# Optimization experiments

Measured on AMD Instinct MI355X. Metric: run time of the kernel, lower is better.

The kernel has to match this reference:

```python
import jax, jax.numpy as jnp
import numpy as np

DIM = 1536
HEADS = 12
HEAD_DIM = DIM // HEADS
EPS = 1e-6
IMG_LEN = 257


def _rmsnorm(x, g):
    var = jnp.mean(jnp.square(x), axis=-1, keepdims=True)
    return x * jax.lax.rsqrt(var + EPS) * g


def _attn(q, k, v):
    # q: [b, Lq, h, d], k/v: [b, Lk, h, d]
    scale = 1.0 / jnp.sqrt(jnp.asarray(HEAD_DIM, q.dtype))
    s = jnp.einsum('bqhd,bkhd->bhqk', q, k) * scale
    p = jax.nn.softmax(s, axis=-1)
    return jnp.einsum('bhqk,bkhd->bqhd', p, v)


def setup_inputs() -> dict:
    key = jax.random.key(0)
    ks = jax.random.split(key, 20)
    w = lambda k: jax.random.normal(k, (DIM, DIM), dtype=jnp.float32) * 0.02
    b = lambda k: jax.random.normal(k, (DIM,), dtype=jnp.float32) * 0.01
    return {
        'x': jax.random.normal(ks[0], (1, 16384, DIM), dtype=jnp.float32),
        'context': jax.random.normal(ks[1], (1, 769, DIM), dtype=jnp.float32),
        'context_lens': jax.random.randint(ks[2], (1,), 0, 512, dtype=jnp.int32),
        'Wq': w(ks[3]), 'bq': b(ks[4]),
        'Wk': w(ks[5]), 'bk': b(ks[6]),
        'Wv': w(ks[7]), 'bv': b(ks[8]),
        'W_addk': w(ks[9]), 'b_addk': b(ks[10]),
        'W_addv': w(ks[11]), 'b_addv': b(ks[12]),
        'Wo': w(ks[13]), 'bo': b(ks[14]),
        'gq': jnp.ones((DIM,), dtype=jnp.float32),
        'gk': jnp.ones((DIM,), dtype=jnp.float32),
        'g_addk': jnp.ones((DIM,), dtype=jnp.float32),
    }


def reference(x, context, context_lens, Wq, bq, Wk, bk, Wv, bv,
              W_addk, b_addk, W_addv, b_addv, Wo, bo, gq, gk, g_addk):
    b_sz, L1, _ = x.shape
    ctx_img = context[:, :IMG_LEN]   # [B, 257, C]
    ctx_txt = context[:, IMG_LEN:]   # [B, L2-257, C]

    q = _rmsnorm(x @ Wq + bq, gq).reshape(b_sz, -1, HEADS, HEAD_DIM)
    k = _rmsnorm(ctx_txt @ Wk + bk, gk).reshape(b_sz, -1, HEADS, HEAD_DIM)
    v = (ctx_txt @ Wv + bv).reshape(b_sz, -1, HEADS, HEAD_DIM)
    k_img = _rmsnorm(ctx_img @ W_addk + b_addk, g_addk).reshape(b_sz, -1, HEADS, HEAD_DIM)
    v_img = (ctx_img @ W_addv + b_addv).reshape(b_sz, -1, HEADS, HEAD_DIM)

    img_x = _attn(q, k_img, v_img).reshape(b_sz, L1, DIM)
    txt_x = _attn(q, k, v).reshape(b_sz, L1, DIM)
    out = (txt_x + img_x) @ Wo + bo
    return out
```

## Files before the change

kernel.cpp:

```cpp
#include <hip/hip_runtime.h>
#include <cstdint>
#include <cstddef>

typedef unsigned short u16;
typedef unsigned int u32;
typedef short bfrag __attribute__((ext_vector_type(8)));
typedef __bf16 yfrag __attribute__((ext_vector_type(8)));
typedef float f4 __attribute__((ext_vector_type(4)));

__device__ __forceinline__ u16 f2bs(float f) {
  union { float f; u32 u; } x; x.f = f;
  u32 r = x.u + 0x7fffu + ((x.u >> 16) & 1u);
  return (u16)(r >> 16);
}
__device__ __forceinline__ float bs2f(u16 s) {
  union { u32 u; float f; } x; x.u = ((u32)s) << 16;
  return x.f;
}
__device__ __forceinline__ u32 cvtpk_bf16(float lo, float hi) {
  u32 d;
  asm("v_cvt_pk_bf16_f32 %0, %1, %2" : "=v"(d) : "v"(lo), "v"(hi));
  return d;
}

template <typename T>
__device__ __forceinline__ auto mfma_sel(T a, T b, f4 c, int)
    -> decltype(__builtin_amdgcn_mfma_f32_16x16x32_bf16(a, b, c, 0, 0, 0)) {
  return __builtin_amdgcn_mfma_f32_16x16x32_bf16(a, b, c, 0, 0, 0);
}
template <typename T>
__device__ __forceinline__ f4 mfma_sel(T a, T b, f4 c, long) {
  yfrag ya = __builtin_bit_cast(yfrag, a);
  yfrag yb = __builtin_bit_cast(yfrag, b);
  return __builtin_amdgcn_mfma_f32_16x16x32_bf16(ya, yb, c, 0, 0, 0);
}
__device__ __forceinline__ f4 MFMA(bfrag a, bfrag b, f4 c) {
  return mfma_sel(a, b, c, 0);
}

__device__ __forceinline__ void gl2lds16(const u16* g, u16* l) {
  __builtin_amdgcn_global_load_lds(
      (__attribute__((address_space(1))) void*)(g),
      (__attribute__((address_space(3))) void*)(l), 16, 0, 0);
}

__global__ __launch_bounds__(256) void cvt2(const float* __restrict__ x,
                                            u16* __restrict__ xbf,
                                            const float* __restrict__ ctx,
                                            u16* __restrict__ ctxb) {
  int i = blockIdx.x * 256 + threadIdx.x;
  const float* src; u16* dst;
  if (i < 3145728) {
    src = x; dst = xbf;
  } else {
    i -= 3145728;
    if (i >= 147648) return;
    src = ctx; dst = ctxb;
  }
  const float4* s4 = (const float4*)src;
  float4 a = s4[(size_t)i * 2];
  float4 b = s4[(size_t)i * 2 + 1];
  uint4 o;
  o.x = cvtpk_bf16(a.x, a.y);
  o.y = cvtpk_bf16(a.z, a.w);
  o.z = cvtpk_bf16(b.x, b.y);
  o.w = cvtpk_bf16(b.z, b.w);
  ((uint4*)dst)[i] = o;
}

__global__ __launch_bounds__(256) void transpose6(
    const float* s0, const float* s1, const float* s2, const float* s3,
    const float* s4, const float* s5, u16* d0, u16* d1, u16* d2, u16* d3,
    u16* d4, u16* d5) {
  const float* src; u16* dst;
  switch (blockIdx.z) {
    case 0: src = s0; dst = d0; break;
    case 1: src = s1; dst = d1; break;
    case 2: src = s2; dst = d2; break;
    case 3: src = s3; dst = d3; break;
    case 4: src = s4; dst = d4; break;
    default: src = s5; dst = d5; break;
  }
  __shared__ float tile[32][33];
  int tx = threadIdx.x, ty = threadIdx.y;
  int bx = blockIdx.x * 32, by = blockIdx.y * 32;
#pragma unroll
  for (int j = 0; j < 4; j++)
    tile[ty + j * 8][tx] = src[(size_t)(by + ty + j * 8) * 1536 + bx + tx];
  __syncthreads();
#pragma unroll
  for (int j = 0; j < 4; j++)
    dst[(size_t)(bx + ty + j * 8) * 1536 + by + tx] = f2bs(tile[tx][ty + j * 8]);
}

__device__ __forceinline__ void gemm256_core(
    const u16* __restrict__ A, const u16* __restrict__ Bt,
    const float* __restrict__ bias, void* __restrict__ outp,
    int Mreal, int ldT, int epi, int bx, int by, u16* As, u16* Bs) {
  const int tid = threadIdx.x;
  const int w = tid >> 6, lane = tid & 63;
  const int quad = lane >> 4, l15 = lane & 15;
  const int wm = w >> 2, wn = w & 3;
  const int m0 = bx * 256, n0 = by * 256;

  f4 acc[8][4];
#pragma unroll
  for (int i = 0; i < 8; i++)
#pragma unroll
    for (int j = 0; j < 4; j++) acc[i][j] = f4{0.f, 0.f, 0.f, 0.f};

  const int rbase = w * 8 + (lane >> 3);
  const int csrc = ((lane & 7) ^ (lane >> 3)) * 8;
  const u16* Ab = A + (size_t)m0 * 1536;
  const u16* Bb = Bt + (size_t)n0 * 1536;

#define STG(Gb, Ls, t)                                                      \
  {                                                                         \
    u16* d_ = (Ls) + ((t) & 1) * 16384;                                     \
    const u16* s_ = (Gb) + (size_t)(t) * 64 + csrc;                         \
    _Pragma("unroll")                                                       \
    for (int j = 0; j < 4; j++)                                             \
      gl2lds16(s_ + (size_t)(j * 64 + rbase) * 1536,                        \
               d_ + (j * 512 + w * 64) * 8);                                \
  }

  STG(Ab, As, 0); STG(Bb, Bs, 0);
  STG(Ab, As, 1); STG(Bb, Bs, 1);

  for (int kt = 0; kt < 24; ++kt) {
    const u16* Asb = As + (kt & 1) * 16384;
    const u16* Bsb = Bs + (kt & 1) * 16384;
    if (kt < 23)
      asm volatile("s_waitcnt vmcnt(8)\n\ts_barrier" ::: "memory");
    else
      asm volatile("s_waitcnt vmcnt(0)\n\ts_barrier" ::: "memory");

    bfrag af[8], bf[4];
#pragma unroll
    for (int nf = 0; nf < 4; nf++) {
      const int R = wn * 64 + nf * 16 + l15;
      bf[nf] = *(const bfrag*)(Bsb + R * 64 + ((quad ^ (R & 7)) * 8));
    }
#pragma unroll
    for (int mf = 0; mf < 8; mf++) {
      const int R = wm * 128 + mf * 16 + l15;
      af[mf] = *(const bfrag*)(Asb + R * 64 + ((quad ^ (R & 7)) * 8));
    }
    __builtin_amdgcn_s_setprio(1);
#pragma unroll
    for (int mf = 0; mf < 8; mf++)
#pragma unroll
      for (int nf = 0; nf < 4; nf++)
        acc[mf][nf] = MFMA(af[mf], bf[nf], acc[mf][nf]);
    __builtin_amdgcn_s_setprio(0);

    bfrag af1[8], bf1[4];
#pragma unroll
    for (int nf = 0; nf < 4; nf++) {
      const int R = wn * 64 + nf * 16 + l15;
      bf1[nf] = *(const bfrag*)(Bsb + R * 64 + (((4 + quad) ^ (R & 7)) * 8));
    }
#pragma unroll
    for (int mf = 0; mf < 8; mf++) {
      const int R = wm * 128 + mf * 16 + l15;
      af1[mf] = *(const bfrag*)(Asb + R * 64 + (((4 + quad) ^ (R & 7)) * 8));
    }
    asm volatile("s_waitcnt lgkmcnt(0)\n\ts_barrier" ::: "memory");
    if (kt < 22) { STG(Ab, As, kt + 2); STG(Bb, Bs, kt + 2); }
    __builtin_amdgcn_s_setprio(1);
#pragma unroll
    for (int mf = 0; mf < 8; mf++)
#pragma unroll
      for (int nf = 0; nf < 4; nf++)
        acc[mf][nf] = MFMA(af1[mf], bf1[nf], acc[mf][nf]);
    __builtin_amdgcn_s_setprio(0);
  }
#undef STG

  float bcol[4];
#pragma unroll
  for (int nf = 0; nf < 4; nf++) bcol[nf] = bias[n0 + wn * 64 + nf * 16 + l15];

  if (epi == 1) {
    u16* dst = (u16*)outp;
#pragma unroll
    for (int mf = 0; mf < 8; mf++)
#pragma unroll
      for (int r = 0; r < 4; r++) {
        int row = m0 + wm * 128 + mf * 16 + quad * 4 + r;
        if (row < Mreal) {
#pragma unroll
          for (int nf = 0; nf < 4; nf++) {
            int col = n0 + wn * 64 + nf * 16 + l15;
            dst[(size_t)col * ldT + row] = f2bs(acc[mf][nf][r] + bcol[nf]);
          }
        }
      }
  } else if (epi == 0) {
    u16* dst = (u16*)outp;
#pragma unroll
    for (int mf = 0; mf < 8; mf++)
#pragma unroll
      for (int r = 0; r < 4; r++) {
        int row = m0 + wm * 128 + mf * 16 + quad * 4 + r;
        if (row < Mreal) {
#pragma unroll
          for (int nf = 0; nf < 4; nf++) {
            int col = n0 + wn * 64 + nf * 16 + l15;
            dst[(size_t)row * 1536 + col] = f2bs(acc[mf][nf][r] + bcol[nf]);
          }
        }
      }
  } else {
    float* dst = (float*)outp;
#pragma unroll
    for (int mf = 0; mf < 8; mf++)
#pragma unroll
      for (int r = 0; r < 4; r++) {
        int row = m0 + wm * 128 + mf * 16 + quad * 4 + r;
        if (row < Mreal) {
#pragma unroll
          for (int nf = 0; nf < 4; nf++) {
            int col = n0 + wn * 64 + nf * 16 + l15;
            dst[(size_t)row * 1536 + col] = acc[mf][nf][r] + bcol[nf];
          }
        }
      }
  }
}

__global__ __launch_bounds__(512, 2) void gemm256(
    const u16* __restrict__ xbf, const u16* __restrict__ wqT,
    const float* __restrict__ bq, u16* __restrict__ qb,
    const u16* __restrict__ ctxb, const u16* __restrict__ wkT,
    const float* __restrict__ bk, u16* __restrict__ ktxt,
    const u16* __restrict__ wakT, const float* __restrict__ bak,
    u16* __restrict__ kimg, const u16* __restrict__ wvT,
    const float* __restrict__ bv, u16* __restrict__ vtt,
    const u16* __restrict__ wavT, const float* __restrict__ bav,
    u16* __restrict__ vti, const u16* __restrict__ yb,
    const u16* __restrict__ woT, const float* __restrict__ bo,
    float* __restrict__ out, int mode) {
  extern __shared__ u16 lds[];
  u16* As = lds;
  u16* Bs = lds + 32768;
  const int cpx = gridDim.x >> 3;
  int id = (blockIdx.x & 7) * cpx + (blockIdx.x >> 3);
  const u16* ctxt = ctxb + 257 * 1536;
  const u16* A; const u16* Bt; const float* bias; void* outp;
  int Mreal, ldT, epi, bx, by;
  if (mode == 1) {
    A = yb; Bt = woT; bias = bo; outp = out;
    Mreal = 16384; ldT = 0; epi = 2; bx = id & 63; by = id >> 6;
  } else if (id < 384) {
    A = xbf; Bt = wqT; bias = bq; outp = qb;
    Mreal = 16384; ldT = 0; epi = 0; bx = id & 63; by = id >> 6;
  } else if (id < 396) {
    int t = id - 384;
    A = ctxt; Bt = wkT; bias = bk; outp = ktxt;
    Mreal = 512; ldT = 0; epi = 0; bx = t & 1; by = t >> 1;
  } else if (id < 408) {
    int t = id - 396;
    A = ctxb; Bt = wakT; bias = bak; outp = kimg;
    Mreal = 257; ldT = 0; epi = 0; bx = t & 1; by = t >> 1;
  } else if (id < 420) {
    int t = id - 408;
    A = ctxt; Bt = wvT; bias = bv; outp = vtt;
    Mreal = 512; ldT = 512; epi = 1; bx = t & 1; by = t >> 1;
  } else {
    int t = id - 420;
    A = ctxb; Bt = wavT; bias = bav; outp = vti;
    Mreal = 257; ldT = 264; epi = 1; bx = t & 1; by = t >> 1;
  }
  gemm256_core(A, Bt, bias, outp, Mreal, ldT, epi, bx, by, As, Bs);
}

__global__ __launch_bounds__(256) void rmsnorm_multi(
    u16* __restrict__ qb, const float* __restrict__ gq,
    u16* __restrict__ ktxt, const float* __restrict__ gk,
    u16* __restrict__ kimg, const float* __restrict__ gak) {
  int row = blockIdx.x;
  u16* buf; const float* g;
  if (row < 16384) {
    buf = qb; g = gq;
  } else if (row < 16896) {
    buf = ktxt; g = gk; row -= 16384;
  } else {
    buf = kimg; g = gak; row -= 16896;
  }
  const int tid = threadIdx.x;
  u32* p = (u32*)(buf + (size_t)row * 1536);
  const float2* g2 = (const float2*)g;
  u32 d[3];
  float v[6];
  float ss = 0.f;
#pragma unroll
  for (int j = 0; j < 3; j++) {
    d[j] = p[tid + j * 256];
    v[2 * j]     = bs2f((u16)(d[j] & 0xffffu));
    v[2 * j + 1] = bs2f((u16)(d[j] >> 16));
    ss += v[2 * j] * v[2 * j] + v[2 * j + 1] * v[2 * j + 1];
  }
#pragma unroll
  for (int off = 32; off; off >>= 1) ss += __shfl_xor(ss, off);
  __shared__ float red[4];
  if ((tid & 63) == 0) red[tid >> 6] = ss;
  __syncthreads();
  ss = red[0] + red[1] + red[2] + red[3];
  const float sc = rsqrtf(ss * (1.0f / 1536.0f) + 1e-6f);
#pragma unroll
  for (int j = 0; j < 3; j++) {
    float2 gg = g2[tid + j * 256];
    p[tid + j * 256] =
        cvtpk_bf16(v[2 * j] * sc * gg.x, v[2 * j + 1] * sc * gg.y);
  }
}

#define ATTN_SCALE 0.08838834764831845f
__global__ __launch_bounds__(256, 2) void attn_kernel(
    const u16* __restrict__ q, const u16* __restrict__ ktxt,
    const u16* __restrict__ kimg, const u16* __restrict__ vttxt,
    const u16* __restrict__ vtimg, u16* __restrict__ y) {
  __shared__ u16 Ks[64 * 128];
  __shared__ u16 Vs[128 * 64];
  __shared__ u16 Ps[4 * 32 * 72];
  const int tid = threadIdx.x;
  const int w = tid >> 6, lane = tid & 63;
  const int quad = lane >> 4, l15 = lane & 15;
  const int h = blockIdx.y, hoff = h * 128;
  const int mw = blockIdx.x * 128 + w * 32;
  u16* Pw = Ps + w * (32 * 72);

  bfrag qf[2][4];
#pragma unroll
  for (int rt = 0; rt < 2; rt++) {
    const u16* qrow = q + (size_t)(mw + rt * 16 + l15) * 1536 + hoff + quad * 8;
#pragma unroll
    for (int c = 0; c < 4; c++) qf[rt][c] = *(const bfrag*)(qrow + c * 32);
  }

  int kko[4], kco[4], vfe[4], vco[4];
#pragma unroll
  for (int j = 0; j < 4; j++) {
    int i = j * 256 + tid;
    int s = i >> 4, cp = i & 15;
    kko[j] = 4 * (s & 15) + (s >> 4);
    kco[j] = ((cp ^ (s & 7)) * 8);
    int f = i >> 3, cq = i & 7;
    vfe[j] = f;
    vco[j] = ((cq ^ (f & 7)) * 8);
  }

  f4 o[2][8];
  u32 resA[2][8][2];
  float lr[2][4];

  for (int seg = 0; seg < 2; seg++) {
    const u16* kp = seg ? ktxt : kimg;
    const u16* vp = seg ? vttxt : vtimg;
    const int Lk = seg ? 512 : 257;
    const int ldv = seg ? 512 : 264;
    const int nit = seg ? 8 : 5;
#pragma unroll
    for (int rt = 0; rt < 2; rt++) {
#pragma unroll
      for (int ft = 0; ft < 8; ft++) o[rt][ft] = f4{0.f, 0.f, 0.f, 0.f};
#pragma unroll
      for (int r = 0; r < 4; r++) lr[rt][r] = 0.f;
    }

    for (int it = 0; it < nit; ++it) {
      const int t0 = it * 64;
#pragma unroll
      for (int j = 0; j < 4; j++)
        gl2lds16(kp + (size_t)(t0 + kko[j]) * 1536 + hoff + kco[j],
                 Ks + (j * 256 + w * 64) * 8);
#pragma unroll
      for (int j = 0; j < 4; j++)
        gl2lds16(vp + (size_t)(hoff + vfe[j]) * ldv + t0 + vco[j],
                 Vs + (j * 256 + w * 64) * 8);
      __syncthreads();

      f4 s[2][4];
#pragma unroll
      for (int rt = 0; rt < 2; rt++)
#pragma unroll
        for (int t = 0; t < 4; t++) s[rt][t] = f4{0.f, 0.f, 0.f, 0.f};
#pragma unroll
      for (int t = 0; t < 4; t++) {
        const u16* kb = Ks + (t * 16 + l15) * 128;
        bfrag kf[4];
#pragma unroll
        for (int c = 0; c < 4; c++)
          kf[c] = *(const bfrag*)(kb + (((c * 4 + quad) ^ (l15 & 7)) * 8));
#pragma unroll
        for (int rt = 0; rt < 2; rt++)
#pragma unroll
          for (int c = 0; c < 4; c++)
            s[rt][t] = MFMA(qf[rt][c], kf[c], s[rt][t]);
      }

      if (t0 + 64 <= Lk) {
#pragma unroll
        for (int rt = 0; rt < 2; rt++)
#pragma unroll
          for (int t = 0; t < 4; t++)
#pragma unroll
            for (int r = 0; r < 4; r++) {
              float p = __expf(s[rt][t][r] * ATTN_SCALE);
              s[rt][t][r] = p;
              lr[rt][r] += p;
            }
      } else {
#pragma unroll
        for (int t = 0; t < 4; t++) {
          bool ok = (t0 + 4 * l15 + t) < Lk;
#pragma unroll
          for (int rt = 0; rt < 2; rt++)
#pragma unroll
            for (int r = 0; r < 4; r++) {
              float p = ok ? __expf(s[rt][t][r] * ATTN_SCALE) : 0.f;
              s[rt][t][r] = p;
              lr[rt][r] += p;
            }
        }
      }

#pragma unroll
      for (int rt = 0; rt < 2; rt++)
#pragma unroll
        for (int r = 0; r < 4; r++) {
          u32 lo = cvtpk_bf16(s[rt][0][r], s[rt][1][r]);
          u32 hi = cvtpk_bf16(s[rt][2][r], s[rt][3][r]);
          *(uint2*)(Pw + (rt * 16 + quad * 4 + r) * 72 + l15 * 4) =
              make_uint2(lo, hi);
        }
      asm volatile("s_waitcnt lgkmcnt(0)" ::: "memory");
      bfrag pf[2][2];
#pragma unroll
      for (int rt = 0; rt < 2; rt++)
#pragma unroll
        for (int hf = 0; hf < 2; hf++)
          pf[rt][hf] =
              *(const bfrag*)(Pw + (rt * 16 + l15) * 72 + hf * 32 + quad * 8);

#pragma unroll
      for (int ft = 0; ft < 8; ft++) {
        const u16* vb = Vs + (ft * 16 + l15) * 64;
#pragma unroll
        for (int hf = 0; hf < 2; hf++) {
          bfrag vf = *(const bfrag*)(vb + (((hf * 4 + quad) ^ (l15 & 7)) * 8));
#pragma unroll
          for (int rt = 0; rt < 2; rt++)
            o[rt][ft] = MFMA(pf[rt][hf], vf, o[rt][ft]);
        }
      }
      __syncthreads();
    }

#pragma unroll
    for (int rt = 0; rt < 2; rt++)
#pragma unroll
      for (int r = 0; r < 4; r++) {
        float v = lr[rt][r];
        v += __shfl_xor(v, 1);
        v += __shfl_xor(v, 2);
        v += __shfl_xor(v, 4);
        v += __shfl_xor(v, 8);
        lr[rt][r] = 1.0f / v;
      }
    if (seg == 0) {
#pragma unroll
      for (int rt = 0; rt < 2; rt++)
#pragma unroll
        for (int ft = 0; ft < 8; ft++) {
          resA[rt][ft][0] = cvtpk_bf16(o[rt][ft][0] * lr[rt][0],
                                       o[rt][ft][1] * lr[rt][1]);
          resA[rt][ft][1] = cvtpk_bf16(o[rt][ft][2] * lr[rt][2],
                                       o[rt][ft][3] * lr[rt][3]);
        }
    }
  }

#pragma unroll
  for (int rt = 0; rt < 2; rt++)
#pragma unroll
    for (int ft = 0; ft < 8; ft++) {
      float ra[4];
      ra[0] = bs2f((u16)(resA[rt][ft][0] & 0xffffu));
      ra[1] = bs2f((u16)(resA[rt][ft][0] >> 16));
      ra[2] = bs2f((u16)(resA[rt][ft][1] & 0xffffu));
      ra[3] = bs2f((u16)(resA[rt][ft][1] >> 16));
#pragma unroll
      for (int r = 0; r < 4; r++)
        y[(size_t)(mw + rt * 16 + quad * 4 + r) * 1536 + hoff + ft * 16 + l15] =
            f2bs(ra[r] + o[rt][ft][r] * lr[rt][r]);
    }
}

extern "C" void kernel_launch(void* const* d_in, const int* in_sizes, int n_in,
                              void* d_out, int out_size, void* d_ws,
                              size_t ws_size, hipStream_t stream) {
  const float* x   = (const float*)d_in[0];
  const float* ctx = (const float*)d_in[1];
  const float* Wq  = (const float*)d_in[3];
  const float* bq  = (const float*)d_in[4];
  const float* Wk  = (const float*)d_in[5];
  const float* bk  = (const float*)d_in[6];
  const float* Wv  = (const float*)d_in[7];
  const float* bv  = (const float*)d_in[8];
  const float* Wak = (const float*)d_in[9];
  const float* bak = (const float*)d_in[10];
  const float* Wav = (const float*)d_in[11];
  const float* bav = (const float*)d_in[12];
  const float* Wo  = (const float*)d_in[13];
  const float* bo  = (const float*)d_in[14];
  const float* gq  = (const float*)d_in[15];
  const float* gk  = (const float*)d_in[16];
  const float* gak = (const float*)d_in[17];
  float* out = (float*)d_out;

  u16* xbf  = (u16*)d_ws;
  u16* qb   = xbf + 25165824;
  u16* ctxb = qb + 25165824;
  u16* wqT  = ctxb + 1181184;
  u16* wkT  = wqT + 2359296;
  u16* wvT  = wkT + 2359296;
  u16* wakT = wvT + 2359296;
  u16* wavT = wakT + 2359296;
  u16* woT  = wavT + 2359296;
  u16* ktxt = woT + 2359296;
  u16* kimg = ktxt + 786432;
  u16* vti  = kimg + 394752;
  u16* vtt  = vti + 405504;

  cvt2<<<12865, 256, 0, stream>>>(x, xbf, ctx, ctxb);
  transpose6<<<dim3(48, 48, 6), dim3(32, 8), 0, stream>>>(
      Wq, Wk, Wv, Wak, Wav, Wo, wqT, wkT, wvT, wakT, wavT, woT);

  gemm256<<<432, 512, 131072, stream>>>(xbf, wqT, bq, qb,
                                        ctxb, wkT, bk, ktxt,
                                        wakT, bak, kimg,
                                        wvT, bv, vtt,
                                        wavT, bav, vti,
                                        xbf, woT, bo, out, 0);

  rmsnorm_multi<<<17153, 256, 0, stream>>>(qb, gq, ktxt, gk, kimg, gak);

  attn_kernel<<<dim3(128, 12), 256, 0, stream>>>(qb, ktxt, kimg, vtt, vti, xbf);

  gemm256<<<384, 512, 131072, stream>>>(xbf, wqT, bq, qb,
                                        ctxb, wkT, bk, ktxt,
                                        wakT, bak, kimg,
                                        wvT, bv, vtt,
                                        wavT, bav, vti,
                                        xbf, woT, bo, out, 1);
}
```

Before: 575.9 us.

## Restructure 256x256 GEMM mainloop into 4-stage BK=32 pipeline with split staging

The GEMM main loop moves from a double-buffered BK=64 scheme to a quadruple-buffered BK=32 scheme with three tiles in flight. A and B global-to-LDS loads are interleaved between two half-MFMA phases, and the LDS layout and swizzle are reorganised to match. The wait and barrier schedule is rewritten per iteration to keep more loads outstanding. Launch bounds drop to one block per SM, which frees registers but may lower occupancy, and the extra barriers per iteration add synchronisation overhead.

Result: slower. 590.6 us (+2.5%).

```diff
diff --git a/kernel.cpp b/kernel.cpp
--- a/kernel.cpp
+++ b/kernel.cpp
@@ -109,71 +109,80 @@
 #pragma unroll
     for (int j = 0; j < 4; j++) acc[i][j] = f4{0.f, 0.f, 0.f, 0.f};
 
-  const int rbase = w * 8 + (lane >> 3);
-  const int csrc = ((lane & 7) ^ (lane >> 3)) * 8;
+  const int g = lane >> 3;
+  const int c_ = (lane & 7) ^ g;
+  const int R0 = (c_ >> 2) * 128 + w * 8 + g;
+  const int qs = (c_ & 3) * 8;
   const u16* Ab = A + (size_t)m0 * 1536;
   const u16* Bb = Bt + (size_t)n0 * 1536;
 
-#define STG(Gb, Ls, t)                                                      \
-  {                                                                         \
-    u16* d_ = (Ls) + ((t) & 1) * 16384;                                     \
-    const u16* s_ = (Gb) + (size_t)(t) * 64 + csrc;                         \
-    _Pragma("unroll")                                                       \
-    for (int j = 0; j < 4; j++)                                             \
-      gl2lds16(s_ + (size_t)(j * 64 + rbase) * 1536,                        \
-               d_ + (j * 512 + w * 64) * 8);                                \
+#define STG(Gb, Ls, t)                                                     \
+  {                                                                        \
+    u16* d_ = (Ls) + ((t) & 3) * 8192;                                     \
+    const u16* s_ = (Gb) + (size_t)(t) * 32 + qs;                          \
+    gl2lds16(s_ + (size_t)R0 * 1536, d_ + (w * 64) * 8);                   \
+    gl2lds16(s_ + (size_t)(R0 + 64) * 1536, d_ + (512 + w * 64) * 8);      \
   }
 
   STG(Ab, As, 0); STG(Bb, Bs, 0);
   STG(Ab, As, 1); STG(Bb, Bs, 1);
-
-  for (int kt = 0; kt < 24; ++kt) {
-    const u16* Asb = As + (kt & 1) * 16384;
-    const u16* Bsb = Bs + (kt & 1) * 16384;
-    if (kt < 23)
-      asm volatile("s_waitcnt vmcnt(8)\n\ts_barrier" ::: "memory");
-    else
-      asm volatile("s_waitcnt vmcnt(0)\n\ts_barrier" ::: "memory");
-
-    bfrag af[8], bf[4];
+  STG(Ab, As, 2); STG(Bb, Bs, 2);
+  asm volatile("s_waitcnt vmcnt(8)" ::: "memory");
+  __builtin_amdgcn_s_barrier();
+
+  for (int kt = 0; kt < 48; ++kt) {
+    const u16* Asb = As + (kt & 3) * 8192;
+    const u16* Bsb = Bs + (kt & 3) * 8192;
+
+    bfrag bf[4], af[4];
 #pragma unroll
     for (int nf = 0; nf < 4; nf++) {
-      const int R = wn * 64 + nf * 16 + l15;
-      bf[nf] = *(const bfrag*)(Bsb + R * 64 + ((quad ^ (R & 7)) * 8));
-    }
-#pragma unroll
-    for (int mf = 0; mf < 8; mf++) {
-      const int R = wm * 128 + mf * 16 + l15;
-      af[mf] = *(const bfrag*)(Asb + R * 64 + ((quad ^ (R & 7)) * 8));
-    }
+      const int br = (wn & 1) * 64 + nf * 16 + l15;
+      bf[nf] = *(const bfrag*)(Bsb + br * 64 +
+                               ((((wn >> 1) * 4 + quad) ^ (br & 7)) * 8));
+    }
+#pragma unroll
+    for (int mf = 0; mf < 4; mf++) {
+      const int ar = mf * 16 + l15;
+      af[mf] = *(const bfrag*)(Asb + ar * 64 +
+                               (((wm * 4 + quad) ^ (ar & 7)) * 8));
+    }
+    if (kt < 45) STG(Ab, As, kt + 3);
+    __builtin_amdgcn_s_barrier();
+    asm volatile("s_waitcnt lgkmcnt(0)" ::: "memory");
     __builtin_amdgcn_s_setprio(1);
 #pragma unroll
-    for (int mf = 0; mf < 8; mf++)
+    for (int mf = 0; mf < 4; mf++)
 #pragma unroll
       for (int nf = 0; nf < 4; nf++)
         acc[mf][nf] = MFMA(af[mf], bf[nf], acc[mf][nf]);
     __builtin_amdgcn_s_setprio(0);
-
-    bfrag af1[8], bf1[4];
-#pragma unroll
-    for (int nf = 0; nf < 4; nf++) {
-      const int R = wn * 64 + nf * 16 + l15;
-      bf1[nf] = *(const bfrag*)(Bsb + R * 64 + (((4 + quad) ^ (R & 7)) * 8));
-    }
-#pragma unroll
-    for (int mf = 0; mf < 8; mf++) {
-      const int R = wm * 128 + mf * 16 + l15;
-      af1[mf] = *(const bfrag*)(Asb + R * 64 + (((4 + quad) ^ (R & 7)) * 8));
-    }
-    asm volatile("s_waitcnt lgkmcnt(0)\n\ts_barrier" ::: "memory");
-    if (kt < 22) { STG(Ab, As, kt + 2); STG(Bb, Bs, kt + 2); }
+    __builtin_amdgcn_s_barrier();
+
+    bfrag af2[4];
+#pragma unroll
+    for (int mf = 0; mf < 4; mf++) {
+      const int ar = (mf + 4) * 16 + l15;
+      af2[mf] = *(const bfrag*)(Asb + ar * 64 +
+                                (((wm * 4 + quad) ^ (ar & 7)) * 8));
+    }
+    if (kt < 45) STG(Bb, Bs, kt + 3);
+    __builtin_amdgcn_s_barrier();
+    asm volatile("s_waitcnt lgkmcnt(0)" ::: "memory");
     __builtin_amdgcn_s_setprio(1);
 #pragma unroll
-    for (int mf = 0; mf < 8; mf++)
+    for (int mf = 0; mf < 4; mf++)
 #pragma unroll
       for (int nf = 0; nf < 4; nf++)
-        acc[mf][nf] = MFMA(af1[mf], bf1[nf], acc[mf][nf]);
+        acc[mf + 4][nf] = MFMA(af2[mf], bf[nf], acc[mf + 4][nf]);
     __builtin_amdgcn_s_setprio(0);
+    if (kt < 45)
+      asm volatile("s_waitcnt vmcnt(8)" ::: "memory");
+    else if (kt == 45)
+      asm volatile("s_waitcnt vmcnt(4)" ::: "memory");
+    else if (kt == 46)
+      asm volatile("s_waitcnt vmcnt(0)" ::: "memory");
+    __builtin_amdgcn_s_barrier();
   }
 #undef STG
 
@@ -229,7 +238,7 @@
   }
 }
 
-__global__ __launch_bounds__(512, 2) void gemm256(
+__global__ __launch_bounds__(512, 1) void gemm256(
     const u16* __restrict__ xbf, const u16* __restrict__ wqT,
     const float* __restrict__ bq, u16* __restrict__ qb,
     const u16* __restrict__ ctxb, const u16* __restrict__ wkT,
```

## Double-buffer K/V tiles in attention and merge prep kernels into one launch

Applied to the files above, without the earlier changes.

The attention kernel now keeps two LDS buffers for K and V and prefetches the next 64-key tile while computing on the current one. The image and text segments are flattened into a single 13-step loop, which removes one barrier per tile and lets loads overlap MFMA work. The P staging buffer is halved to one row tile at a time to offset the extra LDS. The bf16 conversion and weight transpose kernels are fused into one launch, saving a kernel launch. The cost is higher LDS use per block, which could lower occupancy.

Measured after the change: 570.9 us. Within noise of the previous version (-0.9%).

```diff
diff --git a/kernel.cpp b/kernel.cpp
--- a/kernel.cpp
+++ b/kernel.cpp
@@ -44,36 +44,41 @@
       (__attribute__((address_space(3))) void*)(l), 16, 0, 0);
 }
 
-__global__ __launch_bounds__(256) void cvt2(const float* __restrict__ x,
-                                            u16* __restrict__ xbf,
-                                            const float* __restrict__ ctx,
-                                            u16* __restrict__ ctxb) {
-  int i = blockIdx.x * 256 + threadIdx.x;
+__global__ __launch_bounds__(256) void prep(
+    const float* __restrict__ x, u16* __restrict__ xbf,
+    const float* __restrict__ ctx, u16* __restrict__ ctxb,
+    const float* s0, const float* s1, const float* s2, const float* s3,
+    const float* s4, const float* s5, u16* d0, u16* d1, u16* d2,
+    u16* d3, u16* d4, u16* d5) {
+  __shared__ float tile[32][33];
+  const int tid = threadIdx.x;
+  int b = blockIdx.x;
+  if (b < 12865) {
+    int i = b * 256 + tid;
+    const float* src; u16* dst;
+    if (i < 3145728) {
+      src = x; dst = xbf;
+    } else {
+      i -= 3145728;
+      if (i >= 147648) return;
+      src = ctx; dst = ctxb;
+    }
+    const float4* s4p = (const float4*)src;
+    float4 a = s4p[(size_t)i * 2];
+    float4 c = s4p[(size_t)i * 2 + 1];
+    uint4 o;
+    o.x = cvtpk_bf16(a.x, a.y);
+    o.y = cvtpk_bf16(a.z, a.w);
+    o.z = cvtpk_bf16(c.x, c.y);
+    o.w = cvtpk_bf16(c.z, c.w);
+    ((uint4*)dst)[i] = o;
+    return;
+  }
+  b -= 12865;
+  const int z = b / 2304, rem = b % 2304;
+  const int byy = rem / 48, bxx = rem % 48;
   const float* src; u16* dst;
-  if (i < 3145728) {
-    src = x; dst = xbf;
-  } else {
-    i -= 3145728;
-    if (i >= 147648) return;
-    src = ctx; dst = ctxb;
-  }
-  const float4* s4 = (const float4*)src;
-  float4 a = s4[(size_t)i * 2];
-  float4 b = s4[(size_t)i * 2 + 1];
-  uint4 o;
-  o.x = cvtpk_bf16(a.x, a.y);
-  o.y = cvtpk_bf16(a.z, a.w);
-  o.z = cvtpk_bf16(b.x, b.y);
-  o.w = cvtpk_bf16(b.z, b.w);
-  ((uint4*)dst)[i] = o;
-}
-
-__global__ __launch_bounds__(256) void transpose6(
-    const float* s0, const float* s1, const float* s2, const float* s3,
-    const float* s4, const float* s5, u16* d0, u16* d1, u16* d2, u16* d3,
-    u16* d4, u16* d5) {
-  const float* src; u16* dst;
-  switch (blockIdx.z) {
+  switch (z) {
     case 0: src = s0; dst = d0; break;
     case 1: src = s1; dst = d1; break;
     case 2: src = s2; dst = d2; break;
@@ -81,9 +86,8 @@
     case 4: src = s4; dst = d4; break;
     default: src = s5; dst = d5; break;
   }
-  __shared__ float tile[32][33];
-  int tx = threadIdx.x, ty = threadIdx.y;
-  int bx = blockIdx.x * 32, by = blockIdx.y * 32;
+  const int tx = tid & 31, ty = tid >> 5;
+  const int bx = bxx * 32, by = byy * 32;
 #pragma unroll
   for (int j = 0; j < 4; j++)
     tile[ty + j * 8][tx] = src[(size_t)(by + ty + j * 8) * 1536 + bx + tx];
@@ -321,15 +325,15 @@
     const u16* __restrict__ q, const u16* __restrict__ ktxt,
     const u16* __restrict__ kimg, const u16* __restrict__ vttxt,
     const u16* __restrict__ vtimg, u16* __restrict__ y) {
-  __shared__ u16 Ks[64 * 128];
-  __shared__ u16 Vs[128 * 64];
-  __shared__ u16 Ps[4 * 32 * 72];
+  __shared__ u16 Ks[2][64 * 128];
+  __shared__ u16 Vs[2][128 * 64];
+  __shared__ u16 Ps[4 * 16 * 72];
   const int tid = threadIdx.x;
   const int w = tid >> 6, lane = tid & 63;
   const int quad = lane >> 4, l15 = lane & 15;
   const int h = blockIdx.y, hoff = h * 128;
   const int mw = blockIdx.x * 128 + w * 32;
-  u16* Pw = Ps + w * (32 * 72);
+  u16* Pw = Ps + w * (16 * 72);
 
   bfrag qf[2][4];
 #pragma unroll
@@ -354,122 +358,37 @@
   f4 o[2][8];
   u32 resA[2][8][2];
   float lr[2][4];
-
-  for (int seg = 0; seg < 2; seg++) {
-    const u16* kp = seg ? ktxt : kimg;
-    const u16* vp = seg ? vttxt : vtimg;
-    const int Lk = seg ? 512 : 257;
-    const int ldv = seg ? 512 : 264;
-    const int nit = seg ? 8 : 5;
-#pragma unroll
-    for (int rt = 0; rt < 2; rt++) {
-#pragma unroll
-      for (int ft = 0; ft < 8; ft++) o[rt][ft] = f4{0.f, 0.f, 0.f, 0.f};
-#pragma unroll
-      for (int r = 0; r < 4; r++) lr[rt][r] = 0.f;
-    }
-
-    for (int it = 0; it < nit; ++it) {
-      const int t0 = it * 64;
-#pragma unroll
-      for (int j = 0; j < 4; j++)
-        gl2lds16(kp + (size_t)(t0 + kko[j]) * 1536 + hoff + kco[j],
-                 Ks + (j * 256 + w * 64) * 8);
-#pragma unroll
-      for (int j = 0; j < 4; j++)
-        gl2lds16(vp + (size_t)(hoff + vfe[j]) * ldv + t0 + vco[j],
-                 Vs + (j * 256 + w * 64) * 8);
-      __syncthreads();
-
-      f4 s[2][4];
+#pragma unroll
+  for (int rt = 0; rt < 2; rt++) {
+#pragma unroll
+    for (int ft = 0; ft < 8; ft++) o[rt][ft] = f4{0.f, 0.f, 0.f, 0.f};
+#pragma unroll
+    for (int r = 0; r < 4; r++) lr[rt][r] = 0.f;
+  }
+
+#pragma unroll
+  for (int j = 0; j < 4; j++)
+    gl2lds16(kimg + (size_t)kko[j] * 1536 + hoff + kco[j],
+             Ks[0] + (j * 256 + w * 64) * 8);
+#pragma unroll
+  for (int j = 0; j < 4; j++)
+    gl2lds16(vtimg + (size_t)(hoff + vfe[j]) * 264 + vco[j],
+             Vs[0] + (j * 256 + w * 64) * 8);
+  __syncthreads();
+
+  for (int t = 0; t < 13; ++t) {
+    if (t == 5) {
 #pragma unroll
       for (int rt = 0; rt < 2; rt++)
 #pragma unroll
-        for (int t = 0; t < 4; t++) s[rt][t] = f4{0.f, 0.f, 0.f, 0.f};
-#pragma unroll
-      for (int t = 0; t < 4; t++) {
-        const u16* kb = Ks + (t * 16 + l15) * 128;
-        bfrag kf[4];
-#pragma unroll
-        for (int c = 0; c < 4; c++)
-          kf[c] = *(const bfrag*)(kb + (((c * 4 + quad) ^ (l15 & 7)) * 8));
-#pragma unroll
-        for (int rt = 0; rt < 2; rt++)
-#pragma unroll
-          for (int c = 0; c < 4; c++)
-            s[rt][t] = MFMA(qf[rt][c], kf[c], s[rt][t]);
-      }
-
-      if (t0 + 64 <= Lk) {
-#pragma unroll
-        for (int rt = 0; rt < 2; rt++)
-#pragma unroll
-          for (int t = 0; t < 4; t++)
-#pragma unroll
-            for (int r = 0; r < 4; r++) {
-              float p = __expf(s[rt][t][r] * ATTN_SCALE);
-              s[rt][t][r] = p;
-              lr[rt][r] += p;
-            }
-      } else {
-#pragma unroll
-        for (int t = 0; t < 4; t++) {
-          bool ok = (t0 + 4 * l15 + t) < Lk;
-#pragma unroll
-          for (int rt = 0; rt < 2; rt++)
-#pragma unroll
-            for (int r = 0; r < 4; r++) {
-              float p = ok ? __expf(s[rt][t][r] * ATTN_SCALE) : 0.f;
-              s[rt][t][r] = p;
-              lr[rt][r] += p;
-            }
+        for (int r = 0; r < 4; r++) {
+          float v = lr[rt][r];
+          v += __shfl_xor(v, 1);
+          v += __shfl_xor(v, 2);
+          v += __shfl_xor(v, 4);
+          v += __shfl_xor(v, 8);
+          lr[rt][r] = 1.0f / v;
         }
-      }
-
-#pragma unroll
-      for (int rt = 0; rt < 2; rt++)
-#pragma unroll
-        for (int r = 0; r < 4; r++) {
-          u32 lo = cvtpk_bf16(s[rt][0][r], s[rt][1][r]);
-          u32 hi = cvtpk_bf16(s[rt][2][r], s[rt][3][r]);
-          *(uint2*)(Pw + (rt * 16 + quad * 4 + r) * 72 + l15 * 4) =
-              make_uint2(lo, hi);
-        }
-      asm volatile("s_waitcnt lgkmcnt(0)" ::: "memory");
-      bfrag pf[2][2];
-#pragma unroll
-      for (int rt = 0; rt < 2; rt++)
-#pragma unroll
-        for (int hf = 0; hf < 2; hf++)
-          pf[rt][hf] =
-              *(const bfrag*)(Pw + (rt * 16 + l15) * 72 + hf * 32 + quad * 8);
-
-#pragma unroll
-      for (int ft = 0; ft < 8; ft++) {
-        const u16* vb = Vs + (ft * 16 + l15) * 64;
-#pragma unroll
-        for (int hf = 0; hf < 2; hf++) {
-          bfrag vf = *(const bfrag*)(vb + (((hf * 4 + quad) ^ (l15 & 7)) * 8));
-#pragma unroll
-          for (int rt = 0; rt < 2; rt++)
-            o[rt][ft] = MFMA(pf[rt][hf], vf, o[rt][ft]);
-        }
-      }
-      __syncthreads();
-    }
-
-#pragma unroll
-    for (int rt = 0; rt < 2; rt++)
-#pragma unroll
-      for (int r = 0; r < 4; r++) {
-        float v = lr[rt][r];
-        v += __shfl_xor(v, 1);
-        v += __shfl_xor(v, 2);
-        v += __shfl_xor(v, 4);
-        v += __shfl_xor(v, 8);
-        lr[rt][r] = 1.0f / v;
-      }
-    if (seg == 0) {
 #pragma unroll
       for (int rt = 0; rt < 2; rt++)
 #pragma unroll
@@ -478,9 +397,120 @@
                                        o[rt][ft][1] * lr[rt][1]);
           resA[rt][ft][1] = cvtpk_bf16(o[rt][ft][2] * lr[rt][2],
                                        o[rt][ft][3] * lr[rt][3]);
+          o[rt][ft] = f4{0.f, 0.f, 0.f, 0.f};
         }
-    }
-  }
+#pragma unroll
+      for (int rt = 0; rt < 2; rt++)
+#pragma unroll
+        for (int r = 0; r < 4; r++) lr[rt][r] = 0.f;
+    }
+
+    const u16* Kb = Ks[t & 1];
+    const u16* Vb = Vs[t & 1];
+
+    if (t < 12) {
+      const int tn = t + 1;
+      const u16* kp; const u16* vp; int t0n, ldv;
+      if (tn < 5) { kp = kimg; vp = vtimg; t0n = tn * 64; ldv = 264; }
+      else        { kp = ktxt; vp = vttxt; t0n = (tn - 5) * 64; ldv = 512; }
+      u16* Kd = Ks[tn & 1];
+      u16* Vd = Vs[tn & 1];
+#pragma unroll
+      for (int j = 0; j < 4; j++)
+        gl2lds16(kp + (size_t)(t0n + kko[j]) * 1536 + hoff + kco[j],
+                 Kd + (j * 256 + w * 64) * 8);
+#pragma unroll
+      for (int j = 0; j < 4; j++)
+        gl2lds16(vp + (size_t)(hoff + vfe[j]) * ldv + t0n + vco[j],
+                 Vd + (j * 256 + w * 64) * 8);
+    }
+
+    f4 s[2][4];
+#pragma unroll
+    for (int rt = 0; rt < 2; rt++)
+#pragma unroll
+      for (int tt = 0; tt < 4; tt++) s[rt][tt] = f4{0.f, 0.f, 0.f, 0.f};
+#pragma unroll
+    for (int tt = 0; tt < 4; tt++) {
+      const u16* kb = Kb + (tt * 16 + l15) * 128;
+      bfrag kf[4];
+#pragma unroll
+      for (int c = 0; c < 4; c++)
+        kf[c] = *(const bfrag*)(kb + (((c * 4 + quad) ^ (l15 & 7)) * 8));
+#pragma unroll
+      for (int rt = 0; rt < 2; rt++)
+#pragma unroll
+        for (int c = 0; c < 4; c++)
+          s[rt][tt] = MFMA(qf[rt][c], kf[c], s[rt][tt]);
+    }
+
+    if (t != 4) {
+#pragma unroll
+      for (int rt = 0; rt < 2; rt++)
+#pragma unroll
+        for (int tt = 0; tt < 4; tt++)
+#pragma unroll
+          for (int r = 0; r < 4; r++) {
+            float p = __expf(s[rt][tt][r] * ATTN_SCALE);
+            s[rt][tt][r] = p;
+            lr[rt][r] += p;
+          }
+    } else {
+#pragma unroll
+      for (int tt = 0; tt < 4; tt++) {
+        bool ok = (256 + 4 * l15 + tt) < 257;
+#pragma unroll
+        for (int rt = 0; rt < 2; rt++)
+#pragma unroll
+          for (int r = 0; r < 4; r++) {
+            float p = ok ? __expf(s[rt][tt][r] * ATTN_SCALE) : 0.f;
+            s[rt][tt][r] = p;
+            lr[rt][r] += p;
+          }
+      }
+    }
+
+    bfrag pf[2][2];
+#pragma unroll
+    for (int rt = 0; rt < 2; rt++) {
+#pragma unroll
+      for (int r = 0; r < 4; r++) {
+        u32 lo = cvtpk_bf16(s[rt][0][r], s[rt][1][r]);
+        u32 hi = cvtpk_bf16(s[rt][2][r], s[rt][3][r]);
+        *(uint2*)(Pw + (quad * 4 + r) * 72 + l15 * 4) = make_uint2(lo, hi);
+      }
+      asm volatile("s_waitcnt lgkmcnt(0)" ::: "memory");
+#pragma unroll
+      for (int hf = 0; hf < 2; hf++)
+        pf[rt][hf] = *(const bfrag*)(Pw + l15 * 72 + hf * 32 + quad * 8);
+    }
+
+#pragma unroll
+    for (int ft = 0; ft < 8; ft++) {
+      const u16* vb = Vb + (ft * 16 + l15) * 64;
+#pragma unroll
+      for (int hf = 0; hf < 2; hf++) {
+        bfrag vf = *(const bfrag*)(vb + (((hf * 4 + quad) ^ (l15 & 7)) * 8));
+#pragma unroll
+        for (int rt = 0; rt < 2; rt++)
+          o[rt][ft] = MFMA(pf[rt][hf], vf, o[rt][ft]);
+      }
+    }
+
+    __syncthreads();
+  }
+
+#pragma unroll
+  for (int rt = 0; rt < 2; rt++)
+#pragma unroll
+    for (int r = 0; r < 4; r++) {
+      float v = lr[rt][r];
+      v += __shfl_xor(v, 1);
+      v += __shfl_xor(v, 2);
+      v += __shfl_xor(v, 4);
+      v += __shfl_xor(v, 8);
+      lr[rt][r] = 1.0f / v;
+    }
 
 #pragma unroll
   for (int rt = 0; rt < 2; rt++)
@@ -534,9 +564,9 @@
   u16* vti  = kimg + 394752;
   u16* vtt  = vti + 405504;
 
-  cvt2<<<12865, 256, 0, stream>>>(x, xbf, ctx, ctxb);
-  transpose6<<<dim3(48, 48, 6), dim3(32, 8), 0, stream>>>(
-      Wq, Wk, Wv, Wak, Wav, Wo, wqT, wkT, wvT, wakT, wavT, woT);
+  prep<<<26689, 256, 0, stream>>>(x, xbf, ctx, ctxb,
+                                  Wq, Wk, Wv, Wak, Wav, Wo,
+                                  wqT, wkT, wvT, wakT, wavT, woT);
 
   gemm256<<<432, 512, 131072, stream>>>(xbf, wqT, bq, qb,
                                         ctxb, wkT, bk, ktxt,
```
